# Kernel tuning notes

Hardware: AMD Instinct MI355X
Metric: run time of the kernel (lower is better)

Reference implementation:

```python
import jax, jax.numpy as jnp
import numpy as np

N = 20000   # nodes
E = 320000  # edges (before self loops)
T = 32768   # total tokens for BiLSTM/Transformer features
H = 4       # heads
C = 64      # emb_dim per head
NEG_SLOPE = 0.2


def gat_layer(x, W, a_src, a_dst, b, src, dst):
    # x: [N, Fin] -> h: [N, H, C]
    h = (x @ W).reshape(N, H, C)
    al = jnp.einsum('nhc,hc->nh', h, a_src)  # source attention logits
    ar = jnp.einsum('nhc,hc->nh', h, a_dst)  # target attention logits
    e = jax.nn.leaky_relu(al[src] + ar[dst], NEG_SLOPE)  # [Etot, H]
    m = jax.ops.segment_max(e, dst, num_segments=N)      # [N, H]
    ex = jnp.exp(e - m[dst])
    s = jax.ops.segment_sum(ex, dst, num_segments=N)
    alpha = ex / (s[dst] + 1e-16)                         # edge softmax per target
    msg = alpha[:, :, None] * h[src]                      # [Etot, H, C]
    out = jax.ops.segment_sum(msg, dst, num_segments=N)   # aggr='add'
    return out.reshape(N, H * C) + b


def setup_inputs() -> dict:
    key = jax.random.key(0)
    ks = jax.random.split(key, 32)
    s = 0.05
    rn = lambda k, sh, sc=1.0: jax.random.normal(k, sh, dtype=jnp.float32) * sc
    inp = {}
    inp['x'] = rn(ks[0], (N, 128))
    inp['edge_index'] = jax.random.randint(ks[1], (2, E), 0, N, dtype=jnp.int32)
    inp['batch'] = jnp.sort(jax.random.randint(ks[2], (N,), 0, 64, dtype=jnp.int32))
    inp['VOCindex'] = jnp.sort(jax.random.randint(ks[3], (N,), 0, T, dtype=jnp.int32))
    inp['BiLSTM_feature'] = rn(ks[4], (T, 128))
    inp['Transformer_feature'] = rn(ks[5], (T, 128))
    inp['W0'] = rn(ks[6], (128, H * C), s)
    inp['a_src0'] = rn(ks[7], (H, C), s)
    inp['a_dst0'] = rn(ks[8], (H, C), s)
    inp['b0'] = rn(ks[9], (H * C,), s)
    inp['W1'] = rn(ks[10], (H * C, H * C), s)
    inp['a_src1'] = rn(ks[11], (H, C), s)
    inp['a_dst1'] = rn(ks[12], (H, C), s)
    inp['b1'] = rn(ks[13], (H * C,), s)
    inp['W2'] = rn(ks[14], (H * C, H * C), s)
    inp['a_src2'] = rn(ks[15], (H, C), s)
    inp['a_dst2'] = rn(ks[16], (H, C), s)
    inp['b2'] = rn(ks[17], (H * C,), s)
    inp['fcmax_w'] = rn(ks[18], (H * C, H * C), s)
    inp['fcmax_b'] = rn(ks[19], (H * C,), s)
    inp['fc1_w'] = rn(ks[20], (3 * 2 * H * C, 2 * H * C), s)
    inp['fc1_b'] = rn(ks[21], (2 * H * C,), s)
    inp['fc2_w'] = rn(ks[22], (2 * H * C, 2 * C), s)
    inp['fc2_b'] = rn(ks[23], (2 * C,), s)
    inp['fc3_w'] = rn(ks[24], (2 * C, C), s)
    inp['fc3_b'] = rn(ks[25], (C,), s)
    return inp


def reference(x, edge_index, batch, VOCindex, BiLSTM_feature, Transformer_feature,
              W0, a_src0, a_dst0, b0, W1, a_src1, a_dst1, b1, W2, a_src2, a_dst2, b2,
              fcmax_w, fcmax_b, fc1_w, fc1_b, fc2_w, fc2_b, fc3_w, fc3_b):
    loop = jnp.arange(N, dtype=edge_index.dtype)
    src = jnp.concatenate([edge_index[0], loop])  # PyG GATConv adds self-loops
    dst = jnp.concatenate([edge_index[1], loop])
    params = [(W0, a_src0, a_dst0, b0), (W1, a_src1, a_dst1, b1), (W2, a_src2, a_dst2, b2)]
    h = x
    x_all = []
    for (W, asr, ads, b) in params:
        h = gat_layer(h, W, asr, ads, b, src, dst)
        x_all.append(h)
        h = jax.nn.relu(h @ fcmax_w + fcmax_b)
        x_all.append(h)
    z = jnp.concatenate(x_all, axis=1)               # [N, 1536]
    z = jax.nn.relu(z @ fc1_w + fc1_b)
    z = jax.nn.relu(z @ fc2_w + fc2_b)
    gnn_feature = z @ fc3_w + fc3_b                   # [N, C]
    b_sel = BiLSTM_feature[VOCindex]                  # [N, 128]
    t_sel = Transformer_feature[VOCindex]             # [N, 128]
    return (b_sel, t_sel, gnn_feature, batch)
```

## Files before the change

kernel.cpp:

```cpp
#include <hip/hip_runtime.h>
#include <math.h>

#define NN 20000
#define NPAD 20096
#define EE 320000
#define ET (EE + NN)

typedef __attribute__((ext_vector_type(8))) short bf16x8;
typedef __attribute__((ext_vector_type(4))) float f32x4;
typedef __attribute__((ext_vector_type(4))) unsigned short us4;
typedef __attribute__((ext_vector_type(8))) unsigned short us8;
typedef __attribute__((ext_vector_type(4))) float fx4;

__device__ inline unsigned short f2bf(float f) {
    union { float f; unsigned u; } x; x.f = f;
    unsigned u = x.u;
    return (unsigned short)((u + 0x7FFF + ((u >> 16) & 1)) >> 16);
}
__device__ inline float bf2f(unsigned short u) {
    union { unsigned u; float f; } x; x.u = (unsigned)u << 16; return x.f;
}

__device__ inline void storeC(float* C, size_t idx, float v) { C[idx] = v; }
__device__ inline void storeC(unsigned short* C, size_t idx, float v) { C[idx] = f2bf(v); }

__device__ inline void gload_lds16(const void* g, void* l) {
    __builtin_amdgcn_global_load_lds(
        (const __attribute__((address_space(1))) unsigned int*)g,
        (__attribute__((address_space(3))) unsigned int*)l, 16, 0, 0);
}

__global__ __launch_bounds__(256) void transpose_bf16(const float* __restrict__ W,
                                                      unsigned short* __restrict__ Wt,
                                                      int K, int N) {
    __shared__ float t[32][33];
    int k0 = blockIdx.x * 32, n0 = blockIdx.y * 32;
    int c = threadIdx.x & 31, r8 = threadIdx.x >> 5;
    #pragma unroll
    for (int i = 0; i < 4; i++)
        t[r8 + i * 8][c] = W[(size_t)(k0 + r8 + i * 8) * N + n0 + c];
    __syncthreads();
    #pragma unroll
    for (int i = 0; i < 4; i++)
        Wt[(size_t)(n0 + r8 + i * 8) * K + k0 + c] = f2bf(t[c][r8 + i * 8]);
}

__global__ void cvt_bf16_v4(const float* __restrict__ in, unsigned short* __restrict__ out, int n4) {
    int i = blockIdx.x * blockDim.x + threadIdx.x;
    if (i < n4) {
        fx4 v = *(const fx4*)(in + (size_t)i * 4);
        us4 s;
        #pragma unroll
        for (int j = 0; j < 4; j++) s[j] = f2bf(v[j]);
        *(us4*)(out + (size_t)i * 4) = s;
    }
}

__global__ void count_init(int* cnt) {
    int n = blockIdx.x * blockDim.x + threadIdx.x;
    if (n < NN) cnt[n] = 1;
}

__global__ void count_edges(const int* dst, int* cnt) {
    int e = blockIdx.x * blockDim.x + threadIdx.x;
    if (e < EE) atomicAdd(&cnt[dst[e]], 1);
}

__global__ void scan_kernel(const int* cnt, int* indptr, int* cursor) {
    __shared__ int part[1024];
    int tid = threadIdx.x;
    const int CH = 20;
    int base = tid * CH;
    int sum = 0;
    for (int i = 0; i < CH; i++) {
        int idx = base + i;
        if (idx < NN) sum += cnt[idx];
    }
    part[tid] = sum;
    __syncthreads();
    for (int off = 1; off < 1024; off <<= 1) {
        int v = (tid >= off) ? part[tid - off] : 0;
        __syncthreads();
        part[tid] += v;
        __syncthreads();
    }
    int run = (tid == 0) ? 0 : part[tid - 1];
    for (int i = 0; i < CH; i++) {
        int idx = base + i;
        if (idx < NN) {
            indptr[idx] = run;
            cursor[idx] = run;
            run += cnt[idx];
        }
    }
    if (tid == 1023) indptr[NN] = run;
}

__global__ void scatter_self(int* cursor, int* esrc) {
    int n = blockIdx.x * blockDim.x + threadIdx.x;
    if (n < NN) {
        int pos = atomicAdd(&cursor[n], 1);
        esrc[pos] = n;
    }
}

__global__ void scatter_edges(const int* src, const int* dst, int* cursor, int* esrc) {
    int e = blockIdx.x * blockDim.x + threadIdx.x;
    if (e < EE) {
        int pos = atomicAdd(&cursor[dst[e]], 1);
        esrc[pos] = src[e];
    }
}

template <int BN, typename TC>
__global__ __launch_bounds__(256) void mfma_gemm(
    const unsigned short* __restrict__ A, int lda,
    const unsigned short* __restrict__ Bt, int ldbt,
    TC* __restrict__ C, int ldc,
    int M, int K,
    const float* __restrict__ bias, int relu, int nwgx)
{
    constexpr int BM = 128, BK = 64;
    constexpr int NJ = BN / 16;
    constexpr int NCHB = BN / 8;
    __shared__ unsigned short Als[2][BM * BK];
    __shared__ unsigned short Bls[2][BN * BK];

    int nwg = gridDim.x;
    int orig = blockIdx.x;
    int q = nwg >> 3, r = nwg & 7;
    int xcd = orig & 7, loc = orig >> 3;
    int swz = (xcd < r ? xcd * (q + 1) : r * (q + 1) + (xcd - r) * q) + loc;
    int bx = swz % nwgx, by = swz / nwgx;

    int tid = threadIdx.x;
    int lane = tid & 63, w = tid >> 6;
    int row0 = by * BM, col0 = bx * BN;

    int lr = lane >> 3;
    int scol = ((lane & 7) ^ lr) << 3;

    f32x4 acc[2][NJ];
    #pragma unroll
    for (int i = 0; i < 2; i++)
        #pragma unroll
        for (int j = 0; j < NJ; j++) acc[i][j] = (f32x4){0.f, 0.f, 0.f, 0.f};

    auto stage = [&](int buf, int k0) {
        #pragma unroll
        for (int i = 0; i < 4; i++) {
            int ch = (w << 2) + i;
            gload_lds16(A + (size_t)(row0 + (ch << 3) + lr) * lda + k0 + scol,
                        &Als[buf][(ch << 9) + (lane << 3)]);
        }
        #pragma unroll
        for (int i = 0; i < NCHB / 4; i++) {
            int ch = w * (NCHB / 4) + i;
            gload_lds16(Bt + (size_t)(col0 + (ch << 3) + lr) * ldbt + k0 + scol,
                        &Bls[buf][(ch << 9) + (lane << 3)]);
        }
    };

    auto compute = [&](int buf) {
        #pragma unroll
        for (int kc = 0; kc < 2; kc++) {
            int ks = (kc << 2) + (lane >> 4);
            bf16x8 af[2];
            #pragma unroll
            for (int i = 0; i < 2; i++) {
                int rr = (w << 5) + (i << 4) + (lane & 15);
                af[i] = *(bf16x8*)&Als[buf][(rr << 6) + ((ks ^ (rr & 7)) << 3)];
            }
            bf16x8 bfr[NJ];
            #pragma unroll
            for (int j = 0; j < NJ; j++) {
                int rr = (j << 4) + (lane & 15);
                bfr[j] = *(bf16x8*)&Bls[buf][(rr << 6) + ((ks ^ (rr & 7)) << 3)];
            }
            #pragma unroll
            for (int i = 0; i < 2; i++)
                #pragma unroll
                for (int j = 0; j < NJ; j++)
                    acc[i][j] = __builtin_amdgcn_mfma_f32_16x16x32_bf16(af[i], bfr[j], acc[i][j], 0, 0, 0);
        }
    };

    stage(0, 0);
    asm volatile("s_waitcnt vmcnt(0)" ::: "memory");
    __builtin_amdgcn_s_barrier();
    int NT = K >> 6, cur = 0;
    for (int t = 0; t < NT - 1; ++t) {
        stage(cur ^ 1, (t + 1) << 6);
        compute(cur);
        asm volatile("s_waitcnt vmcnt(0)" ::: "memory");
        __builtin_amdgcn_s_barrier();
        cur ^= 1;
    }
    compute(cur);

    #pragma unroll
    for (int i = 0; i < 2; i++) {
        #pragma unroll
        for (int rr = 0; rr < 4; rr++) {
            int row = row0 + w * 32 + i * 16 + ((lane >> 4) << 2) + rr;
            if (row >= M) continue;
            #pragma unroll
            for (int j = 0; j < NJ; j++) {
                int col = col0 + j * 16 + (lane & 15);
                float v = acc[i][j][rr] + (bias ? bias[col] : 0.f);
                if (relu) v = fmaxf(v, 0.f);
                storeC(C, (size_t)row * ldc + col, v);
            }
        }
    }
}

__global__ __launch_bounds__(256) void logits_kernel(
    const unsigned short* __restrict__ hbuf,
    const float* __restrict__ a_src, const float* __restrict__ a_dst,
    float* __restrict__ al, float* __restrict__ ar)
{
    int w = threadIdx.x >> 6;
    int n = blockIdx.x * 4 + w;
    if (n >= NN) return;
    int lane = threadIdx.x & 63;
    int c4 = lane * 4;
    us4 hv = *(const us4*)&hbuf[(size_t)n * 256 + c4];
    fx4 asv = *(const fx4*)&a_src[c4];
    fx4 adv = *(const fx4*)&a_dst[c4];
    float ps = 0.f, pd = 0.f;
    #pragma unroll
    for (int k = 0; k < 4; k++) {
        float h = bf2f(hv[k]);
        ps += h * asv[k];
        pd += h * adv[k];
    }
    #pragma unroll
    for (int off = 8; off; off >>= 1) {
        ps += __shfl_xor(ps, off);
        pd += __shfl_xor(pd, off);
    }
    if ((lane & 15) == 0) {
        al[n * 4 + (lane >> 4)] = ps;
        ar[n * 4 + (lane >> 4)] = pd;
    }
}

__global__ __launch_bounds__(256) void aggregate_kernel(
    const unsigned short* __restrict__ hbuf,
    const float* __restrict__ al, const float* __restrict__ ar,
    const int* __restrict__ indptr, const int* __restrict__ esrc,
    const float* __restrict__ bias,
    unsigned short* __restrict__ out, int ldo)
{
    int w = threadIdx.x >> 6;
    int n = blockIdx.x * 4 + w;
    if (n >= NN) return;
    int lane = threadIdx.x & 63;
    int myh = lane >> 4;
    int c4 = lane * 4;
    int beg = indptr[n], end = indptr[n + 1];

    fx4 arn = *(const fx4*)&ar[(size_t)n * 4];

    fx4 mv = (fx4){-1e30f, -1e30f, -1e30f, -1e30f};
    for (int j = beg + lane; j < end; j += 64) {
        fx4 a = *(const fx4*)&al[(size_t)esrc[j] * 4];
        #pragma unroll
        for (int h = 0; h < 4; h++) {
            float e = a[h] + arn[h];
            e = e > 0.f ? e : 0.2f * e;
            mv[h] = fmaxf(mv[h], e);
        }
    }
    #pragma unroll
    for (int off = 32; off; off >>= 1) {
        #pragma unroll
        for (int h = 0; h < 4; h++) mv[h] = fmaxf(mv[h], __shfl_xor(mv[h], off));
    }
    float m = mv[myh];
    float arh = arn[myh];

    float ssum = 0.f;
    fx4 acc = (fx4){0.f, 0.f, 0.f, 0.f};
    int j = beg;
    for (; j + 4 <= end; j += 4) {
        int s0 = esrc[j], s1 = esrc[j + 1], s2 = esrc[j + 2], s3 = esrc[j + 3];
        us4 h0 = *(const us4*)&hbuf[(size_t)s0 * 256 + c4];
        us4 h1 = *(const us4*)&hbuf[(size_t)s1 * 256 + c4];
        us4 h2 = *(const us4*)&hbuf[(size_t)s2 * 256 + c4];
        us4 h3 = *(const us4*)&hbuf[(size_t)s3 * 256 + c4];
        float a0 = al[(size_t)s0 * 4 + myh];
        float a1 = al[(size_t)s1 * 4 + myh];
        float a2 = al[(size_t)s2 * 4 + myh];
        float a3 = al[(size_t)s3 * 4 + myh];
        float e0 = a0 + arh; e0 = e0 > 0.f ? e0 : 0.2f * e0;
        float e1 = a1 + arh; e1 = e1 > 0.f ? e1 : 0.2f * e1;
        float e2 = a2 + arh; e2 = e2 > 0.f ? e2 : 0.2f * e2;
        float e3 = a3 + arh; e3 = e3 > 0.f ? e3 : 0.2f * e3;
        float x0 = __expf(e0 - m), x1 = __expf(e1 - m);
        float x2 = __expf(e2 - m), x3 = __expf(e3 - m);
        ssum += x0 + x1 + x2 + x3;
        #pragma unroll
        for (int k = 0; k < 4; k++)
            acc[k] += x0 * bf2f(h0[k]) + x1 * bf2f(h1[k])
                    + x2 * bf2f(h2[k]) + x3 * bf2f(h3[k]);
    }
    for (; j < end; j++) {
        int s = esrc[j];
        us4 hv = *(const us4*)&hbuf[(size_t)s * 256 + c4];
        float a = al[(size_t)s * 4 + myh];
        float e = a + arh; e = e > 0.f ? e : 0.2f * e;
        float ex = __expf(e - m);
        ssum += ex;
        #pragma unroll
        for (int k = 0; k < 4; k++) acc[k] += ex * bf2f(hv[k]);
    }

    float inv = 1.f / (ssum + 1e-16f);
    us4 o;
    #pragma unroll
    for (int k = 0; k < 4; k++) o[k] = f2bf(acc[k] * inv + bias[c4 + k]);
    *(us4*)&out[(size_t)n * ldo + c4] = o;
}

__global__ void gather_feats(const float* __restrict__ Bf, const float* __restrict__ Tf,
                             const int* __restrict__ voc, const int* __restrict__ batch,
                             float* __restrict__ out)
{
    int i = blockIdx.x * blockDim.x + threadIdx.x;
    if (i < NN * 128) {
        int n = i >> 7, c = i & 127;
        int t = voc[n];
        out[i] = Bf[(long)t * 128 + c];
        out[(long)NN * 128 + i] = Tf[(long)t * 128 + c];
    }
    if (i < NN) out[(long)NN * 128 * 2 + (long)NN * 64 + i] = (float)batch[i];
}

extern "C" void kernel_launch(void* const* d_in, const int* in_sizes, int n_in,
                              void* d_out, int out_size, void* d_ws, size_t ws_size,
                              hipStream_t stream) {
    const float* x     = (const float*)d_in[0];
    const int*   ei    = (const int*)d_in[1];
    const int*   batch = (const int*)d_in[2];
    const int*   voc   = (const int*)d_in[3];
    const float* Bf    = (const float*)d_in[4];
    const float* Tf    = (const float*)d_in[5];
    const float* W0    = (const float*)d_in[6];
    const float* as0   = (const float*)d_in[7];
    const float* ad0   = (const float*)d_in[8];
    const float* b0    = (const float*)d_in[9];
    const float* W1    = (const float*)d_in[10];
    const float* as1   = (const float*)d_in[11];
    const float* ad1   = (const float*)d_in[12];
    const float* b1    = (const float*)d_in[13];
    const float* W2    = (const float*)d_in[14];
    const float* as2   = (const float*)d_in[15];
    const float* ad2   = (const float*)d_in[16];
    const float* b2    = (const float*)d_in[17];
    const float* fcmax_w = (const float*)d_in[18];
    const float* fcmax_b = (const float*)d_in[19];
    const float* fc1_w = (const float*)d_in[20];
    const float* fc1_b = (const float*)d_in[21];
    const float* fc2_w = (const float*)d_in[22];
    const float* fc2_b = (const float*)d_in[23];
    const float* fc3_w = (const float*)d_in[24];
    const float* fc3_b = (const float*)d_in[25];
    float* out = (float*)d_out;

    char* p = (char*)d_ws;
    unsigned short* xb  = (unsigned short*)p; p += (size_t)NPAD * 128 * 2;
    unsigned short* hbuf= (unsigned short*)p; p += (size_t)NN * 256 * 2;
    unsigned short* z   = (unsigned short*)p; p += (size_t)NPAD * 1536 * 2;
    unsigned short* z1  = (unsigned short*)p; p += (size_t)NPAD * 512 * 2;
    unsigned short* h2  = (unsigned short*)p; p += (size_t)NPAD * 128 * 2;
    unsigned short* w0t = (unsigned short*)p; p += (size_t)128 * 256 * 2;
    unsigned short* w1t = (unsigned short*)p; p += (size_t)256 * 256 * 2;
    unsigned short* w2t = (unsigned short*)p; p += (size_t)256 * 256 * 2;
    unsigned short* wmt = (unsigned short*)p; p += (size_t)256 * 256 * 2;
    unsigned short* f1t = (unsigned short*)p; p += (size_t)1536 * 512 * 2;
    unsigned short* f2t = (unsigned short*)p; p += (size_t)512 * 128 * 2;
    unsigned short* f3t = (unsigned short*)p; p += (size_t)128 * 64 * 2;
    float* al   = (float*)p; p += (size_t)NN * 4 * 4;
    float* ar   = (float*)p; p += (size_t)NN * 4 * 4;
    int* cnt    = (int*)p;   p += (size_t)NN * 4;
    int* cursor = (int*)p;   p += (size_t)NN * 4;
    int* esrc   = (int*)p;   p += (size_t)ET * 4;
    int* indptr = (int*)p;   p += (size_t)(NN + 1) * 4;

    const int* e_src = ei;
    const int* e_dst = ei + EE;

    transpose_bf16<<<dim3(4, 8),  256, 0, stream>>>(W0, w0t, 128, 256);
    transpose_bf16<<<dim3(8, 8),  256, 0, stream>>>(W1, w1t, 256, 256);
    transpose_bf16<<<dim3(8, 8),  256, 0, stream>>>(W2, w2t, 256, 256);
    transpose_bf16<<<dim3(8, 8),  256, 0, stream>>>(fcmax_w, wmt, 256, 256);
    transpose_bf16<<<dim3(48, 16),256, 0, stream>>>(fc1_w, f1t, 1536, 512);
    transpose_bf16<<<dim3(16, 4), 256, 0, stream>>>(fc2_w, f2t, 512, 128);
    transpose_bf16<<<dim3(4, 2),  256, 0, stream>>>(fc3_w, f3t, 128, 64);
    cvt_bf16_v4<<<(NN * 32 + 255) / 256, 256, 0, stream>>>(x, xb, NN * 32);

    count_init<<<(NN + 255) / 256, 256, 0, stream>>>(cnt);
    count_edges<<<(EE + 255) / 256, 256, 0, stream>>>(e_dst, cnt);
    scan_kernel<<<1, 1024, 0, stream>>>(cnt, indptr, cursor);
    scatter_self<<<(NN + 255) / 256, 256, 0, stream>>>(cursor, esrc);
    scatter_edges<<<(EE + 255) / 256, 256, 0, stream>>>(e_src, e_dst, cursor, esrc);

    gather_feats<<<(NN * 128 + 255) / 256, 256, 0, stream>>>(Bf, Tf, voc, batch, out);

    const int MB = NPAD / 128;
    const int NB4 = (NN + 3) / 4;

    mfma_gemm<64, unsigned short><<<4 * MB, 256, 0, stream>>>(xb, 128, w0t, 128, hbuf, 256, NN, 128, nullptr, 0, 4);
    logits_kernel<<<NB4, 256, 0, stream>>>(hbuf, as0, ad0, al, ar);
    aggregate_kernel<<<NB4, 256, 0, stream>>>(hbuf, al, ar, indptr, esrc, b0, z + 0, 1536);
    mfma_gemm<64, unsigned short><<<4 * MB, 256, 0, stream>>>(z + 0, 1536, wmt, 256, z + 256, 1536, NN, 256, fcmax_b, 1, 4);

    mfma_gemm<64, unsigned short><<<4 * MB, 256, 0, stream>>>(z + 256, 1536, w1t, 256, hbuf, 256, NN, 256, nullptr, 0, 4);
    logits_kernel<<<NB4, 256, 0, stream>>>(hbuf, as1, ad1, al, ar);
    aggregate_kernel<<<NB4, 256, 0, stream>>>(hbuf, al, ar, indptr, esrc, b1, z + 512, 1536);
    mfma_gemm<64, unsigned short><<<4 * MB, 256, 0, stream>>>(z + 512, 1536, wmt, 256, z + 768, 1536, NN, 256, fcmax_b, 1, 4);

    mfma_gemm<64, unsigned short><<<4 * MB, 256, 0, stream>>>(z + 768, 1536, w2t, 256, hbuf, 256, NN, 256, nullptr, 0, 4);
    logits_kernel<<<NB4, 256, 0, stream>>>(hbuf, as2, ad2, al, ar);
    aggregate_kernel<<<NB4, 256, 0, stream>>>(hbuf, al, ar, indptr, esrc, b2, z + 1024, 1536);
    mfma_gemm<64, unsigned short><<<4 * MB, 256, 0, stream>>>(z + 1024, 1536, wmt, 256, z + 1280, 1536, NN, 256, fcmax_b, 1, 4);

    mfma_gemm<128, unsigned short><<<4 * MB, 256, 0, stream>>>(z, 1536, f1t, 1536, z1, 512, NN, 1536, fc1_b, 1, 4);
    mfma_gemm<64, unsigned short><<<2 * MB, 256, 0, stream>>>(z1, 512, f2t, 512, h2, 128, NN, 512, fc2_b, 1, 2);
    mfma_gemm<64, float><<<1 * MB, 256, 0, stream>>>(h2, 128, f3t, 128, out + (size_t)2 * NN * 128, 64, NN, 128, fc3_b, 0, 1);
}
```

Measured before the change: 368.8 us.

## Add single-shot small-K GEMM, deeper prefetch pipeline, and vectorized feature gather

Adds a single-shot 64x64 GEMM kernel that loads the whole K (128 or 256) into LDS at once, removing the k-loop and double-buffer barriers. It replaces the small-K GEMMs and doubles the number of workgroups, which should give better occupancy on the many CUs. The general GEMM now prefetches two stages ahead and uses partial vmcnt waits so loads overlap with compute. The feature gather is vectorized to float4. Risks are the larger LDS footprint per block and the extra barriers added to the pipelined GEMM.

```diff
diff --git a/kernel.cpp b/kernel.cpp
--- a/kernel.cpp
+++ b/kernel.cpp
@@ -28,6 +28,12 @@
     __builtin_amdgcn_global_load_lds(
         (const __attribute__((address_space(1))) unsigned int*)g,
         (__attribute__((address_space(3))) unsigned int*)l, 16, 0, 0);
+}
+
+__device__ inline int xcd_swz(int orig, int nwg) {
+    int q = nwg >> 3, r = nwg & 7;
+    int xcd = orig & 7, loc = orig >> 3;
+    return (xcd < r ? xcd * (q + 1) : r * (q + 1) + (xcd - r) * q) + loc;
 }
 
 __global__ __launch_bounds__(256) void transpose_bf16(const float* __restrict__ W,
@@ -109,6 +115,76 @@
     if (e < EE) {
         int pos = atomicAdd(&cursor[dst[e]], 1);
         esrc[pos] = src[e];
+    }
+}
+
+template <int KTOT, typename TC>
+__global__ __launch_bounds__(256) void sshot_gemm(
+    const unsigned short* __restrict__ A, int lda,
+    const unsigned short* __restrict__ Bt, int ldbt,
+    TC* __restrict__ C, int ldc,
+    int M, const float* __restrict__ bias, int relu, int nwgx)
+{
+    constexpr int LPR = KTOT / 8;
+    constexpr int RPC = 512 / KTOT;
+    constexpr int NCH = KTOT / 8;
+    constexpr int NCHW = NCH / 4;
+    constexpr int KC = KTOT / 32;
+    __shared__ unsigned short Als[64 * KTOT];
+    __shared__ unsigned short Bls[64 * KTOT];
+
+    int swz = xcd_swz(blockIdx.x, gridDim.x);
+    int bx = swz % nwgx, by = swz / nwgx;
+    int row0 = by * 64, col0 = bx * 64;
+
+    int tid = threadIdx.x;
+    int lane = tid & 63, w = tid >> 6;
+    int ric = lane / LPR, slot = lane % LPR;
+
+    #pragma unroll
+    for (int i = 0; i < NCHW; i++) {
+        int ch = w * NCHW + i;
+        int r = ch * RPC + ric;
+        gload_lds16(A + (size_t)(row0 + r) * lda + ((slot ^ (r & 7)) << 3),
+                    &Als[ch * 512 + lane * 8]);
+    }
+    #pragma unroll
+    for (int i = 0; i < NCHW; i++) {
+        int ch = w * NCHW + i;
+        int r = ch * RPC + ric;
+        gload_lds16(Bt + (size_t)(col0 + r) * ldbt + ((slot ^ (r & 7)) << 3),
+                    &Bls[ch * 512 + lane * 8]);
+    }
+    __syncthreads();
+
+    f32x4 acc[4];
+    #pragma unroll
+    for (int j = 0; j < 4; j++) acc[j] = (f32x4){0.f, 0.f, 0.f, 0.f};
+
+    #pragma unroll
+    for (int kc = 0; kc < KC; kc++) {
+        int ks = (kc << 2) + (lane >> 4);
+        int ra = (w << 4) + (lane & 15);
+        bf16x8 af = *(bf16x8*)&Als[ra * KTOT + ((ks ^ (ra & 7)) << 3)];
+        #pragma unroll
+        for (int j = 0; j < 4; j++) {
+            int rb = (j << 4) + (lane & 15);
+            bf16x8 bf = *(bf16x8*)&Bls[rb * KTOT + ((ks ^ (rb & 7)) << 3)];
+            acc[j] = __builtin_amdgcn_mfma_f32_16x16x32_bf16(af, bf, acc[j], 0, 0, 0);
+        }
+    }
+
+    #pragma unroll
+    for (int rr = 0; rr < 4; rr++) {
+        int row = row0 + (w << 4) + ((lane >> 4) << 2) + rr;
+        if (row >= M) continue;
+        #pragma unroll
+        for (int j = 0; j < 4; j++) {
+            int col = col0 + j * 16 + (lane & 15);
+            float v = acc[j][rr] + (bias ? bias[col] : 0.f);
+            if (relu) v = fmaxf(v, 0.f);
+            storeC(C, (size_t)row * ldc + col, v);
+        }
     }
 }
 
@@ -123,14 +199,11 @@
     constexpr int BM = 128, BK = 64;
     constexpr int NJ = BN / 16;
     constexpr int NCHB = BN / 8;
+    constexpr int PER_STAGE = 4 + NCHB / 4;
     __shared__ unsigned short Als[2][BM * BK];
     __shared__ unsigned short Bls[2][BN * BK];
 
-    int nwg = gridDim.x;
-    int orig = blockIdx.x;
-    int q = nwg >> 3, r = nwg & 7;
-    int xcd = orig & 7, loc = orig >> 3;
-    int swz = (xcd < r ? xcd * (q + 1) : r * (q + 1) + (xcd - r) * q) + loc;
+    int swz = xcd_swz(blockIdx.x, gridDim.x);
     int bx = swz % nwgx, by = swz / nwgx;
 
     int tid = threadIdx.x;
@@ -185,18 +258,21 @@
         }
     };
 
+    int NT = K >> 6;
     stage(0, 0);
-    asm volatile("s_waitcnt vmcnt(0)" ::: "memory");
-    __builtin_amdgcn_s_barrier();
-    int NT = K >> 6, cur = 0;
-    for (int t = 0; t < NT - 1; ++t) {
-        stage(cur ^ 1, (t + 1) << 6);
-        compute(cur);
-        asm volatile("s_waitcnt vmcnt(0)" ::: "memory");
+    stage(1, BK);
+    for (int t = 0; t < NT; ++t) {
+        if (t < NT - 1)
+            asm volatile("s_waitcnt vmcnt(%0)" :: "i"(PER_STAGE) : "memory");
+        else
+            asm volatile("s_waitcnt vmcnt(0)" ::: "memory");
         __builtin_amdgcn_s_barrier();
-        cur ^= 1;
-    }
-    compute(cur);
+        compute(t & 1);
+        if (t + 2 < NT) {
+            __builtin_amdgcn_s_barrier();
+            stage(t & 1, (t + 2) << 6);
+        }
+    }
 
     #pragma unroll
     for (int i = 0; i < 2; i++) {
@@ -329,13 +405,13 @@
                              float* __restrict__ out)
 {
     int i = blockIdx.x * blockDim.x + threadIdx.x;
-    if (i < NN * 128) {
-        int n = i >> 7, c = i & 127;
+    if (i < NN * 32) {
+        int n = i >> 5, c4 = (i & 31) * 4;
         int t = voc[n];
-        out[i] = Bf[(long)t * 128 + c];
-        out[(long)NN * 128 + i] = Tf[(long)t * 128 + c];
-    }
-    if (i < NN) out[(long)NN * 128 * 2 + (long)NN * 64 + i] = (float)batch[i];
+        *(fx4*)&out[(size_t)n * 128 + c4] = *(const fx4*)&Bf[(size_t)t * 128 + c4];
+        *(fx4*)&out[(size_t)NN * 128 + (size_t)n * 128 + c4] = *(const fx4*)&Tf[(size_t)t * 128 + c4];
+    }
+    if (i < NN) out[(size_t)NN * 128 * 2 + (size_t)NN * 64 + i] = (float)batch[i];
 }
 
 extern "C" void kernel_launch(void* const* d_in, const int* in_sizes, int n_in,
@@ -407,27 +483,28 @@
     scatter_self<<<(NN + 255) / 256, 256, 0, stream>>>(cursor, esrc);
     scatter_edges<<<(EE + 255) / 256, 256, 0, stream>>>(e_src, e_dst, cursor, esrc);
 
-    gather_feats<<<(NN * 128 + 255) / 256, 256, 0, stream>>>(Bf, Tf, voc, batch, out);
+    gather_feats<<<(NN * 32 + 255) / 256, 256, 0, stream>>>(Bf, Tf, voc, batch, out);
 
     const int MB = NPAD / 128;
+    const int SB = NPAD / 64;
     const int NB4 = (NN + 3) / 4;
 
-    mfma_gemm<64, unsigned short><<<4 * MB, 256, 0, stream>>>(xb, 128, w0t, 128, hbuf, 256, NN, 128, nullptr, 0, 4);
+    sshot_gemm<128, unsigned short><<<4 * SB, 256, 0, stream>>>(xb, 128, w0t, 128, hbuf, 256, NN, nullptr, 0, 4);
     logits_kernel<<<NB4, 256, 0, stream>>>(hbuf, as0, ad0, al, ar);
     aggregate_kernel<<<NB4, 256, 0, stream>>>(hbuf, al, ar, indptr, esrc, b0, z + 0, 1536);
-    mfma_gemm<64, unsigned short><<<4 * MB, 256, 0, stream>>>(z + 0, 1536, wmt, 256, z + 256, 1536, NN, 256, fcmax_b, 1, 4);
-
-    mfma_gemm<64, unsigned short><<<4 * MB, 256, 0, stream>>>(z + 256, 1536, w1t, 256, hbuf, 256, NN, 256, nullptr, 0, 4);
+    sshot_gemm<256, unsigned short><<<4 * SB, 256, 0, stream>>>(z + 0, 1536, wmt, 256, z + 256, 1536, NN, fcmax_b, 1, 4);
+
+    sshot_gemm<256, unsigned short><<<4 * SB, 256, 0, stream>>>(z + 256, 1536, w1t, 256, hbuf, 256, NN, nullptr, 0, 4);
     logits_kernel<<<NB4, 256, 0, stream>>>(hbuf, as1, ad1, al, ar);
     aggregate_kernel<<<NB4, 256, 0, stream>>>(hbuf, al, ar, indptr, esrc, b1, z + 512, 1536);
-    mfma_gemm<64, unsigned short><<<4 * MB, 256, 0, stream>>>(z + 512, 1536, wmt, 256, z + 768, 1536, NN, 256, fcmax_b, 1, 4);
-
-    mfma_gemm<64, unsigned short><<<4 * MB, 256, 0, stream>>>(z + 768, 1536, w2t, 256, hbuf, 256, NN, 256, nullptr, 0, 4);
+    sshot_gemm<256, unsigned short><<<4 * SB, 256, 0, stream>>>(z + 512, 1536, wmt, 256, z + 768, 1536, NN, fcmax_b, 1, 4);
+
+    sshot_gemm<256, unsigned short><<<4 * SB, 256, 0, stream>>>(z + 768, 1536, w2t, 256, hbuf, 256, NN, nullptr, 0, 4);
     logits_kernel<<<NB4, 256, 0, stream>>>(hbuf, as2, ad2, al, ar);
     aggregate_kernel<<<NB4, 256, 0, stream>>>(hbuf, al, ar, indptr, esrc, b2, z + 1024, 1536);
-    mfma_gemm<64, unsigned short><<<4 * MB, 256, 0, stream>>>(z + 1024, 1536, wmt, 256, z + 1280, 1536, NN, 256, fcmax_b, 1, 4);
+    sshot_gemm<256, unsigned short><<<4 * SB, 256, 0, stream>>>(z + 1024, 1536, wmt, 256, z + 1280, 1536, NN, fcmax_b, 1, 4);
 
     mfma_gemm<128, unsigned short><<<4 * MB, 256, 0, stream>>>(z, 1536, f1t, 1536, z1, 512, NN, 1536, fc1_b, 1, 4);
     mfma_gemm<64, unsigned short><<<2 * MB, 256, 0, stream>>>(z1, 512, f2t, 512, h2, 128, NN, 512, fc2_b, 1, 2);
-    mfma_gemm<64, float><<<1 * MB, 256, 0, stream>>>(h2, 128, f3t, 128, out + (size_t)2 * NN * 128, 64, NN, 128, fc3_b, 0, 1);
-}
+    sshot_gemm<128, float><<<1 * SB, 256, 0, stream>>>(h2, 128, f3t, 128, out + (size_t)2 * NN * 128, 64, NN, fc3_b, 0, 1);
+}
```

Measured after the change: 377.5 us. 2.4% more time.
